# Performance work log

Hardware: AMD Instinct MI355X
Metric: run time of the kernel (lower is better)

Reference implementation:

```python
import jax, jax.numpy as jnp
import numpy as np

B, S, E, H = 32, 256, 768, 32
D = E // H  # head_dim = 24


def setup_inputs() -> dict:
    key = jax.random.key(0)
    ks = jax.random.split(key, 10)
    w_sc = 1.0 / np.sqrt(E)  # xavier-ish init scale for weights
    return {
        "feats": jax.random.normal(ks[0], (B, S, E), jnp.float32),
        "attn_bias": jax.random.normal(ks[1], (B, H, S, S), jnp.float32),
        "delta_pos": jax.random.normal(ks[2], (B, S, S, 3), jnp.float32),
        "Wq": jax.random.normal(ks[3], (E, E), jnp.float32) * w_sc,
        "bq": jnp.zeros((E,), jnp.float32),
        "Wk": jax.random.normal(ks[4], (E, E), jnp.float32) * w_sc,
        "bk": jnp.zeros((E,), jnp.float32),
        "Wv": jax.random.normal(ks[5], (E, E), jnp.float32) * w_sc,
        "bv": jnp.zeros((E,), jnp.float32),
        "Wfx": jax.random.normal(ks[6], (E,), jnp.float32) * w_sc,
        "Wfy": jax.random.normal(ks[7], (E,), jnp.float32) * w_sc,
        "Wfz": jax.random.normal(ks[8], (E,), jnp.float32) * w_sc,
    }


def reference(feats, attn_bias, delta_pos, Wq, bq, Wk, bk, Wv, bv, Wfx, Wfy, Wfz):
    b, s, e = feats.shape
    h = attn_bias.shape[1]
    d = e // h
    scaling = d ** -0.5
    # q/k/v projections; q scaled by 1/sqrt(head_dim)
    q = ((feats @ Wq + bq) * scaling).reshape(b, s, h, d).transpose(0, 2, 1, 3)  # (b,h,s,d)
    k = (feats @ Wk + bk).reshape(b, s, h, d).transpose(0, 2, 1, 3)              # (b,h,t,d)
    v = (feats @ Wv + bv).reshape(b, s, h, d).transpose(0, 2, 1, 3)              # (b,h,t,d)
    scores = jnp.einsum('bhsd,bhtd->bhst', q, k) + attn_bias
    probs = jax.nn.softmax(scores, axis=-1)  # dropout p in eval -> identity
    # rot_attn_probs = probs[...,None] * delta_pos[:,None] fused into one contraction:
    # (b,h,s,t) * (b,s,t,3) contracted with (b,h,t,c) over t -> (b,s,3,h,c)
    attn = jnp.einsum('bhst,bstx,bhtc->bsxhc', probs, delta_pos, v)
    attn = attn.reshape(b, s, 3, e)  # flatten (h,c) -> e
    out_x = attn[..., 0, :] @ Wfx  # (b,s)
    out_y = attn[..., 1, :] @ Wfy
    out_z = attn[..., 2, :] @ Wfz
    return jnp.stack([out_x, out_y, out_z], axis=-1)  # (b,s,3)
```

## Files before the change

kernel.cpp:

```cpp
#include <hip/hip_runtime.h>
#include <hip/hip_bf16.h>

#define B_ 32
#define S_ 256
#define E_ 768
#define H_ 32
#define D_ 24
#define NTOT 1664
#define LK 40

typedef __hip_bfloat16 bf16;
typedef __attribute__((ext_vector_type(8))) short short8;
typedef __attribute__((ext_vector_type(4))) float floatx4;
typedef __attribute__((ext_vector_type(2))) float f32x2;

__global__ __launch_bounds__(256) void cast_feats(
    const float* __restrict__ in, bf16* __restrict__ outp, int n4)
{
  int i = blockIdx.x * 256 + threadIdx.x;
  if (i < n4) {
    float4 v = reinterpret_cast<const float4*>(in)[i];
    union { ushort4 u; bf16 b[4]; } pk;
    pk.b[0] = (bf16)v.x; pk.b[1] = (bf16)v.y;
    pk.b[2] = (bf16)v.z; pk.b[3] = (bf16)v.w;
    reinterpret_cast<ushort4*>(outp)[i] = pk.u;
  }
}

__global__ __launch_bounds__(256) void prep_pack(
    const float* __restrict__ Wq, const float* __restrict__ Wk,
    const float* __restrict__ Wv,
    const float* __restrict__ bq, const float* __restrict__ bk,
    const float* __restrict__ bv,
    const float* __restrict__ Wfx, const float* __restrict__ Wfy,
    const float* __restrict__ Wfz,
    bf16* __restrict__ Wt, float* __restrict__ biasf)
{
  const float qscale = 0.20412414523193154f;
  int gid = blockIdx.x * 256 + threadIdx.x;
  if (gid < NTOT * E_) {
    int n = gid / E_, k = gid % E_;
    float val;
    if (n < 768) {
      val = Wq[(size_t)k * E_ + n] * qscale;
    } else if (n < 1536) {
      val = Wk[(size_t)k * E_ + (n - 768)];
    } else if (n < 1632) {
      int nn = n - 1536, x = nn >> 5, h = nn & 31;
      const float* Wf = (x == 0) ? Wfx : (x == 1 ? Wfy : Wfz);
      float s = 0.f;
      #pragma unroll
      for (int c = 0; c < D_; c++)
        s += Wv[(size_t)k * E_ + h * D_ + c] * Wf[h * D_ + c];
      val = s;
    } else {
      val = 0.f;
    }
    Wt[gid] = (bf16)val;
  } else {
    int n = gid - NTOT * E_;
    if (n < NTOT) {
      float val;
      if (n < 768) {
        val = bq[n] * qscale;
      } else if (n < 1536) {
        val = bk[n - 768];
      } else if (n < 1632) {
        int nn = n - 1536, x = nn >> 5, h = nn & 31;
        const float* Wf = (x == 0) ? Wfx : (x == 1 ? Wfy : Wfz);
        float s = 0.f;
        #pragma unroll
        for (int c = 0; c < D_; c++)
          s += bv[h * D_ + c] * Wf[h * D_ + c];
        val = s;
      } else {
        val = 0.f;
      }
      biasf[n] = val;
    }
  }
}

__global__ __launch_bounds__(256) void gemm_qkv(
    const bf16* __restrict__ A, const bf16* __restrict__ Wt,
    const float* __restrict__ biasf,
    bf16* __restrict__ qout, bf16* __restrict__ kout,
    float* __restrict__ vwout)
{
  __shared__ __align__(16) short As[128 * LK];
  __shared__ __align__(16) short Bs[128 * LK];
  int tid = threadIdx.x;
  int m0 = blockIdx.y * 128, n0 = blockIdx.x * 128;
  int lrow = tid >> 2, lcol = (tid & 3) * 8;
  int wave = tid >> 6, lane = tid & 63;
  int wm = (wave >> 1) * 64, wn = (wave & 1) * 64;
  int fr = lane & 15, quad = lane >> 4;

  floatx4 acc[4][4];
  const floatx4 zero = {0.f, 0.f, 0.f, 0.f};
  #pragma unroll
  for (int i = 0; i < 4; i++)
    #pragma unroll
    for (int j = 0; j < 4; j++) acc[i][j] = zero;

  const bf16* Aptr = A + (size_t)(m0 + lrow) * E_ + lcol;
  const bf16* Bptr = Wt + (size_t)(n0 + lrow) * E_ + lcol;
  float4 av0 = *reinterpret_cast<const float4*>(Aptr);
  float4 av1 = *reinterpret_cast<const float4*>(Aptr + (size_t)64 * E_);
  float4 bv0 = *reinterpret_cast<const float4*>(Bptr);
  float4 bv1 = *reinterpret_cast<const float4*>(Bptr + (size_t)64 * E_);

  for (int k0 = 0; k0 < E_; k0 += 32) {
    __syncthreads();
    *reinterpret_cast<float4*>(&As[lrow * LK + lcol]) = av0;
    *reinterpret_cast<float4*>(&As[(lrow + 64) * LK + lcol]) = av1;
    *reinterpret_cast<float4*>(&Bs[lrow * LK + lcol]) = bv0;
    *reinterpret_cast<float4*>(&Bs[(lrow + 64) * LK + lcol]) = bv1;
    __syncthreads();
    if (k0 + 32 < E_) {
      av0 = *reinterpret_cast<const float4*>(Aptr + k0 + 32);
      av1 = *reinterpret_cast<const float4*>(Aptr + (size_t)64 * E_ + k0 + 32);
      bv0 = *reinterpret_cast<const float4*>(Bptr + k0 + 32);
      bv1 = *reinterpret_cast<const float4*>(Bptr + (size_t)64 * E_ + k0 + 32);
    }
    short8 af[4], bfr[4];
    #pragma unroll
    for (int t = 0; t < 4; t++)
      af[t] = *reinterpret_cast<const short8*>(
          &As[(wm + t * 16 + fr) * LK + quad * 8]);
    #pragma unroll
    for (int t = 0; t < 4; t++)
      bfr[t] = *reinterpret_cast<const short8*>(
          &Bs[(wn + t * 16 + fr) * LK + quad * 8]);
    #pragma unroll
    for (int ti = 0; ti < 4; ti++)
      #pragma unroll
      for (int tj = 0; tj < 4; tj++)
        acc[ti][tj] = __builtin_amdgcn_mfma_f32_16x16x32_bf16(
            af[ti], bfr[tj], acc[ti][tj], 0, 0, 0);
  }

  #pragma unroll
  for (int ti = 0; ti < 4; ti++) {
    #pragma unroll
    for (int tj = 0; tj < 4; tj++) {
      int n = n0 + wn + tj * 16 + fr;
      float bias = biasf[n];
      #pragma unroll
      for (int r = 0; r < 4; r++) {
        int m = m0 + wm + ti * 16 + quad * 4 + r;
        int b = m >> 8, s = m & 255;
        float val = acc[ti][tj][r] + bias;
        if (n < 768) {
          int h = n / 24, d = n - h * 24;
          qout[(((size_t)b * H_ + h) * S_ + s) * D_ + d] = (bf16)val;
        } else if (n < 1536) {
          int n2 = n - 768;
          int h = n2 / 24, d = n2 - h * 24;
          kout[(((size_t)b * H_ + h) * S_ + s) * D_ + d] = (bf16)val;
        } else if (n < 1632) {
          int nn = n - 1536, x = nn >> 5, h = nn & 31;
          vwout[(((size_t)x * B_ + b) * H_ + h) * S_ + s] = val;
        }
      }
    }
  }
}

__global__ __launch_bounds__(256) void attn_kernel(
    const bf16* __restrict__ qg, const bf16* __restrict__ kg,
    const float* __restrict__ vwg, const float* __restrict__ biasg,
    const float* __restrict__ dpg, float* __restrict__ part)
{
  __shared__ __align__(16) float ql[64 * 26];
  int blk = blockIdx.x;
  int b = blk & 31;
  int u = blk >> 5;
  int h = u & 31;
  int st = (u >> 5) * 64;
  int bh = b * H_ + h;
  int tid = threadIdx.x, wave = tid >> 6, lane = tid & 63;
  int t0 = lane * 4;

  f32x2 kr[4][12];
  {
    const short8* kp = reinterpret_cast<const short8*>(
        kg + ((size_t)bh * S_ + t0) * D_);
    #pragma unroll
    for (int v = 0; v < 12; v++) {
      short8 kk = kp[v];
      int row = v / 3, seg = v % 3;
      #pragma unroll
      for (int p2 = 0; p2 < 4; p2++) {
        union { short u; bf16 bb; } a, c;
        a.u = kk[2 * p2]; c.u = kk[2 * p2 + 1];
        f32x2 t2; t2.x = (float)a.bb; t2.y = (float)c.bb;
        kr[row][seg * 4 + p2] = t2;
      }
    }
  }
  float vwr[3][4];
  #pragma unroll
  for (int x = 0; x < 3; x++) {
    float4 v4 = *reinterpret_cast<const float4*>(
        vwg + (((size_t)x * B_ + b) * H_ + h) * S_ + t0);
    vwr[x][0] = v4.x; vwr[x][1] = v4.y; vwr[x][2] = v4.z; vwr[x][3] = v4.w;
  }
  {
    int r = tid >> 2, c0 = (tid & 3) * 6;
    const bf16* qrow = qg + ((size_t)bh * S_ + st + r) * D_ + c0;
    #pragma unroll
    for (int i = 0; i < 6; i++) ql[r * 26 + c0 + i] = (float)qrow[i];
  }
  __syncthreads();

  const float* biasbh = biasg + (size_t)bh * S_ * S_;
  const float* dpb    = dpg + (size_t)b * S_ * S_ * 3;

  float4 nb, nd0, nd1, nd2;
  {
    int s0 = st + wave;
    nb = *reinterpret_cast<const float4*>(biasbh + (size_t)s0 * S_ + t0);
    const float* dpr = dpb + (size_t)s0 * S_ * 3 + (size_t)t0 * 3;
    nd0 = *reinterpret_cast<const float4*>(dpr);
    nd1 = *reinterpret_cast<const float4*>(dpr + 4);
    nd2 = *reinterpret_cast<const float4*>(dpr + 8);
  }

  for (int si = 0; si < 16; si++) {
    float4 bias4 = nb, e0 = nd0, e1 = nd1, e2 = nd2;
    int nsi = (si + 1 < 16) ? si + 1 : 0;
    int ns = st + nsi * 4 + wave;
    nb = *reinterpret_cast<const float4*>(biasbh + (size_t)ns * S_ + t0);
    const float* dpn = dpb + (size_t)ns * S_ * 3 + (size_t)t0 * 3;
    nd0 = *reinterpret_cast<const float4*>(dpn);
    nd1 = *reinterpret_cast<const float4*>(dpn + 4);
    nd2 = *reinterpret_cast<const float4*>(dpn + 8);

    int sr = si * 4 + wave;
    int s  = st + sr;

    f32x2 sc2[4];
    #pragma unroll
    for (int j = 0; j < 4; j++) { sc2[j].x = 0.f; sc2[j].y = 0.f; }
    #pragma unroll
    for (int i = 0; i < 12; i++) {
      f32x2 qd = *reinterpret_cast<const f32x2*>(&ql[sr * 26 + 2 * i]);
      #pragma unroll
      for (int j = 0; j < 4; j++) sc2[j] += qd * kr[j][i];
    }
    float p[4];
    p[0] = __expf(sc2[0].x + sc2[0].y + bias4.x - 4.0f);
    p[1] = __expf(sc2[1].x + sc2[1].y + bias4.y - 4.0f);
    p[2] = __expf(sc2[2].x + sc2[2].y + bias4.z - 4.0f);
    p[3] = __expf(sc2[3].x + sc2[3].y + bias4.w - 4.0f);
    float l = (p[0] + p[1]) + (p[2] + p[3]);

    float dx[4] = {e0.x, e0.w, e1.z, e2.y};
    float dy[4] = {e0.y, e1.x, e1.w, e2.z};
    float dz[4] = {e0.z, e1.y, e2.x, e2.w};

    float ax = 0.f, ay = 0.f, az = 0.f;
    #pragma unroll
    for (int j = 0; j < 4; j++) {
      ax = fmaf(p[j] * dx[j], vwr[0][j], ax);
      ay = fmaf(p[j] * dy[j], vwr[1][j], ay);
      az = fmaf(p[j] * dz[j], vwr[2][j], az);
    }
    #pragma unroll
    for (int o = 32; o; o >>= 1) {
      ax += __shfl_xor(ax, o);
      ay += __shfl_xor(ay, o);
      az += __shfl_xor(az, o);
      l  += __shfl_xor(l, o);
    }
    if (lane == 0) {
      float inv = 1.0f / l;
      float* op = part + ((size_t)bh * S_ + s) * 3;
      op[0] = ax * inv; op[1] = ay * inv; op[2] = az * inv;
    }
  }
}

__global__ __launch_bounds__(256) void reduce_h(
    const float* __restrict__ part, float* __restrict__ out)
{
  int k = blockIdx.x * 256 + threadIdx.x;
  int b = k / (S_ * 3);
  int r = k - b * (S_ * 3);
  const float* p = part + (size_t)b * H_ * S_ * 3 + r;
  float acc = 0.f;
  #pragma unroll
  for (int h = 0; h < H_; h++) acc += p[(size_t)h * S_ * 3];
  out[k] = acc;
}

extern "C" void kernel_launch(void* const* d_in, const int* in_sizes, int n_in,
                              void* d_out, int out_size, void* d_ws, size_t ws_size,
                              hipStream_t stream)
{
  const float* feats     = (const float*)d_in[0];
  const float* attn_bias = (const float*)d_in[1];
  const float* delta_pos = (const float*)d_in[2];
  const float* Wq        = (const float*)d_in[3];
  const float* bq        = (const float*)d_in[4];
  const float* Wk        = (const float*)d_in[5];
  const float* bk        = (const float*)d_in[6];
  const float* Wv        = (const float*)d_in[7];
  const float* bv        = (const float*)d_in[8];
  const float* Wfx       = (const float*)d_in[9];
  const float* Wfy       = (const float*)d_in[10];
  const float* Wfz       = (const float*)d_in[11];

  char* ws = (char*)d_ws;
  size_t off = 0;
  auto alloc = [&](size_t bytes) -> void* {
    void* p = ws + off;
    off = (off + bytes + 255) & ~(size_t)255;
    return p;
  };
  bf16*  ws_fb   = (bf16*) alloc((size_t)B_ * S_ * E_ * 2);
  bf16*  ws_q    = (bf16*) alloc((size_t)B_ * H_ * S_ * D_ * 2);
  bf16*  ws_k    = (bf16*) alloc((size_t)B_ * H_ * S_ * D_ * 2);
  float* ws_vw   = (float*)alloc((size_t)3 * B_ * H_ * S_ * 4);
  bf16*  ws_Wt   = (bf16*) alloc((size_t)NTOT * E_ * 2);
  float* ws_bias = (float*)alloc((size_t)NTOT * 4);
  float* ws_part = (float*)alloc((size_t)B_ * H_ * S_ * 3 * 4);

  int n4 = B_ * S_ * E_ / 4;
  cast_feats<<<(n4 + 255) / 256, 256, 0, stream>>>(feats, ws_fb, n4);

  int prep_n = NTOT * E_ + NTOT;
  prep_pack<<<(prep_n + 255) / 256, 256, 0, stream>>>(
      Wq, Wk, Wv, bq, bk, bv, Wfx, Wfy, Wfz, ws_Wt, ws_bias);

  gemm_qkv<<<dim3(NTOT / 128, B_ * S_ / 128), 256, 0, stream>>>(
      ws_fb, ws_Wt, ws_bias, ws_q, ws_k, ws_vw);

  attn_kernel<<<B_ * H_ * 4, 256, 0, stream>>>(ws_q, ws_k, ws_vw, attn_bias,
                                               delta_pos, ws_part);

  reduce_h<<<(B_ * S_ * 3) / 256, 256, 0, stream>>>(ws_part, (float*)d_out);
}
```

Baseline: 540.0 us.

## Tile-transpose Q/K weight prep, store Q/K row-major, double-buffer bias/delta prefetch

Splits weight packing into a shared-memory tiled transpose kernel for Wq/Wk and a smaller kernel for the fused V·Wf columns and biases, replacing strided uncoalesced reads. The GEMM epilogue now writes Q and K in (b,s,e) layout so stores are contiguous, and the attention kernel reads per-head K rows with a strided row gather. The attention loop is fully unrolled with a two-deep prefetch of attn_bias and delta_pos to hide more global latency, at the cost of extra registers.

```diff
diff --git a/kernel.cpp b/kernel.cpp
--- a/kernel.cpp
+++ b/kernel.cpp
@@ -27,8 +27,33 @@
   }
 }
 
-__global__ __launch_bounds__(256) void prep_pack(
+__global__ __launch_bounds__(256) void prep_qk(
     const float* __restrict__ Wq, const float* __restrict__ Wk,
+    bf16* __restrict__ Wt)
+{
+  __shared__ float tile[64][65];
+  int n0 = blockIdx.x * 64;
+  int k0 = blockIdx.y * 64;
+  int j = threadIdx.x & 63, i4 = threadIdx.x >> 6;
+  const float qscale = 0.20412414523193154f;
+  bool isq = (n0 < 768);
+  const float* W = isq ? Wq : Wk;
+  int nc = isq ? n0 : n0 - 768;
+  float sc = isq ? qscale : 1.0f;
+  #pragma unroll
+  for (int r = 0; r < 16; r++) {
+    int i = r * 4 + i4;
+    tile[i][j] = W[(size_t)(k0 + i) * E_ + nc + j] * sc;
+  }
+  __syncthreads();
+  #pragma unroll
+  for (int r = 0; r < 16; r++) {
+    int jj = r * 4 + i4;
+    Wt[(size_t)(n0 + jj) * E_ + k0 + j] = (bf16)tile[j][jj];
+  }
+}
+
+__global__ __launch_bounds__(256) void prep_vw_bias(
     const float* __restrict__ Wv,
     const float* __restrict__ bq, const float* __restrict__ bk,
     const float* __restrict__ bv,
@@ -38,27 +63,19 @@
 {
   const float qscale = 0.20412414523193154f;
   int gid = blockIdx.x * 256 + threadIdx.x;
-  if (gid < NTOT * E_) {
-    int n = gid / E_, k = gid % E_;
-    float val;
-    if (n < 768) {
-      val = Wq[(size_t)k * E_ + n] * qscale;
-    } else if (n < 1536) {
-      val = Wk[(size_t)k * E_ + (n - 768)];
-    } else if (n < 1632) {
+  if (gid < 128 * E_) {
+    int n = 1536 + gid / E_, k = gid % E_;
+    float val = 0.f;
+    if (n < 1632) {
       int nn = n - 1536, x = nn >> 5, h = nn & 31;
       const float* Wf = (x == 0) ? Wfx : (x == 1 ? Wfy : Wfz);
-      float s = 0.f;
       #pragma unroll
       for (int c = 0; c < D_; c++)
-        s += Wv[(size_t)k * E_ + h * D_ + c] * Wf[h * D_ + c];
-      val = s;
-    } else {
-      val = 0.f;
-    }
-    Wt[gid] = (bf16)val;
+        val += Wv[(size_t)k * E_ + h * D_ + c] * Wf[h * D_ + c];
+    }
+    Wt[(size_t)n * E_ + k] = (bf16)val;
   } else {
-    int n = gid - NTOT * E_;
+    int n = gid - 128 * E_;
     if (n < NTOT) {
       float val;
       if (n < 768) {
@@ -152,15 +169,12 @@
         int b = m >> 8, s = m & 255;
         float val = acc[ti][tj][r] + bias;
         if (n < 768) {
-          int h = n / 24, d = n - h * 24;
-          qout[(((size_t)b * H_ + h) * S_ + s) * D_ + d] = (bf16)val;
+          qout[(size_t)(b * S_ + s) * E_ + n] = (bf16)val;
         } else if (n < 1536) {
-          int n2 = n - 768;
-          int h = n2 / 24, d = n2 - h * 24;
-          kout[(((size_t)b * H_ + h) * S_ + s) * D_ + d] = (bf16)val;
+          kout[(size_t)(b * S_ + s) * E_ + (n - 768)] = (bf16)val;
         } else if (n < 1632) {
-          int nn = n - 1536, x = nn >> 5, h = nn & 31;
-          vwout[(((size_t)x * B_ + b) * H_ + h) * S_ + s] = val;
+          int nn = n - 1536, x = nn >> 5, hh = nn & 31;
+          vwout[(((size_t)x * B_ + b) * H_ + hh) * S_ + s] = val;
         }
       }
     }
@@ -183,19 +197,19 @@
   int t0 = lane * 4;
 
   f32x2 kr[4][12];
-  {
+  #pragma unroll
+  for (int j = 0; j < 4; j++) {
     const short8* kp = reinterpret_cast<const short8*>(
-        kg + ((size_t)bh * S_ + t0) * D_);
-    #pragma unroll
-    for (int v = 0; v < 12; v++) {
-      short8 kk = kp[v];
-      int row = v / 3, seg = v % 3;
+        kg + (size_t)(b * S_ + t0 + j) * E_ + h * D_);
+    #pragma unroll
+    for (int seg = 0; seg < 3; seg++) {
+      short8 kk = kp[seg];
       #pragma unroll
       for (int p2 = 0; p2 < 4; p2++) {
         union { short u; bf16 bb; } a, c;
         a.u = kk[2 * p2]; c.u = kk[2 * p2 + 1];
         f32x2 t2; t2.x = (float)a.bb; t2.y = (float)c.bb;
-        kr[row][seg * 4 + p2] = t2;
+        kr[j][seg * 4 + p2] = t2;
       }
     }
   }
@@ -208,7 +222,7 @@
   }
   {
     int r = tid >> 2, c0 = (tid & 3) * 6;
-    const bf16* qrow = qg + ((size_t)bh * S_ + st + r) * D_ + c0;
+    const bf16* qrow = qg + (size_t)(b * S_ + st + r) * E_ + h * D_ + c0;
     #pragma unroll
     for (int i = 0; i < 6; i++) ql[r * 26 + c0 + i] = (float)qrow[i];
   }
@@ -217,25 +231,28 @@
   const float* biasbh = biasg + (size_t)bh * S_ * S_;
   const float* dpb    = dpg + (size_t)b * S_ * S_ * 3;
 
-  float4 nb, nd0, nd1, nd2;
-  {
-    int s0 = st + wave;
-    nb = *reinterpret_cast<const float4*>(biasbh + (size_t)s0 * S_ + t0);
+  float4 pb[2], pe0[2], pe1[2], pe2[2];
+  #pragma unroll
+  for (int w = 0; w < 2; w++) {
+    int s0 = st + w * 4 + wave;
+    pb[w] = *reinterpret_cast<const float4*>(biasbh + (size_t)s0 * S_ + t0);
     const float* dpr = dpb + (size_t)s0 * S_ * 3 + (size_t)t0 * 3;
-    nd0 = *reinterpret_cast<const float4*>(dpr);
-    nd1 = *reinterpret_cast<const float4*>(dpr + 4);
-    nd2 = *reinterpret_cast<const float4*>(dpr + 8);
-  }
-
+    pe0[w] = *reinterpret_cast<const float4*>(dpr);
+    pe1[w] = *reinterpret_cast<const float4*>(dpr + 4);
+    pe2[w] = *reinterpret_cast<const float4*>(dpr + 8);
+  }
+
+  #pragma unroll
   for (int si = 0; si < 16; si++) {
-    float4 bias4 = nb, e0 = nd0, e1 = nd1, e2 = nd2;
-    int nsi = (si + 1 < 16) ? si + 1 : 0;
+    const int cur = si & 1;
+    float4 bias4 = pb[cur], e0 = pe0[cur], e1 = pe1[cur], e2 = pe2[cur];
+    int nsi = (si + 2 < 16) ? si + 2 : 0;
     int ns = st + nsi * 4 + wave;
-    nb = *reinterpret_cast<const float4*>(biasbh + (size_t)ns * S_ + t0);
+    pb[cur] = *reinterpret_cast<const float4*>(biasbh + (size_t)ns * S_ + t0);
     const float* dpn = dpb + (size_t)ns * S_ * 3 + (size_t)t0 * 3;
-    nd0 = *reinterpret_cast<const float4*>(dpn);
-    nd1 = *reinterpret_cast<const float4*>(dpn + 4);
-    nd2 = *reinterpret_cast<const float4*>(dpn + 8);
+    pe0[cur] = *reinterpret_cast<const float4*>(dpn);
+    pe1[cur] = *reinterpret_cast<const float4*>(dpn + 4);
+    pe2[cur] = *reinterpret_cast<const float4*>(dpn + 8);
 
     int sr = si * 4 + wave;
     int s  = st + sr;
@@ -320,8 +337,8 @@
     return p;
   };
   bf16*  ws_fb   = (bf16*) alloc((size_t)B_ * S_ * E_ * 2);
-  bf16*  ws_q    = (bf16*) alloc((size_t)B_ * H_ * S_ * D_ * 2);
-  bf16*  ws_k    = (bf16*) alloc((size_t)B_ * H_ * S_ * D_ * 2);
+  bf16*  ws_q    = (bf16*) alloc((size_t)B_ * S_ * E_ * 2);
+  bf16*  ws_k    = (bf16*) alloc((size_t)B_ * S_ * E_ * 2);
   float* ws_vw   = (float*)alloc((size_t)3 * B_ * H_ * S_ * 4);
   bf16*  ws_Wt   = (bf16*) alloc((size_t)NTOT * E_ * 2);
   float* ws_bias = (float*)alloc((size_t)NTOT * 4);
@@ -330,9 +347,11 @@
   int n4 = B_ * S_ * E_ / 4;
   cast_feats<<<(n4 + 255) / 256, 256, 0, stream>>>(feats, ws_fb, n4);
 
-  int prep_n = NTOT * E_ + NTOT;
-  prep_pack<<<(prep_n + 255) / 256, 256, 0, stream>>>(
-      Wq, Wk, Wv, bq, bk, bv, Wfx, Wfy, Wfz, ws_Wt, ws_bias);
+  prep_qk<<<dim3(24, 12), 256, 0, stream>>>(Wq, Wk, ws_Wt);
+
+  int prep_n = 128 * E_ + NTOT;
+  prep_vw_bias<<<(prep_n + 255) / 256, 256, 0, stream>>>(
+      Wv, bq, bk, bv, Wfx, Wfy, Wfz, ws_Wt, ws_bias);
 
   gemm_qkv<<<dim3(NTOT / 128, B_ * S_ / 128), 256, 0, stream>>>(
       ws_fb, ws_Wt, ws_bias, ws_q, ws_k, ws_vw);
```

Result: no change. 537.7 us (-0.4%).
